# Kernel tuning notes

Hardware: AMD Instinct MI355X
Metric: run time of the kernel (lower is better)

## Reference

```python
import jax, jax.numpy as jnp
import numpy as np

B, S, D = 16, 512, 384
MAX_DUR = 16  # durations drawn from [0, 16)


def setup_inputs() -> dict:
    key = jax.random.key(0)
    k1, k2 = jax.random.split(key)
    hidden = jax.random.normal(k1, (B, S, D), dtype=jnp.float32)
    durations = jax.random.randint(k2, (B, S), 0, MAX_DUR, dtype=jnp.int32)
    return {"hidden": hidden, "durations": durations}


def reference(hidden, durations):
    # hidden: [B, S, D], durations: [B, S] int
    out_lengths = durations.sum(axis=1)              # [B]
    # NOTE: output length is data-dependent (matches torch eager semantics);
    # concretize it here. Under jit one would pass a static max_length instead.
    max_length = int(out_lengths.max())
    csum = jnp.cumsum(durations, axis=1)             # [B, S] inclusive cumsum
    pos = jnp.arange(max_length)                     # [L]
    # Output frame j of batch b copies token t where csum[b,t-1] <= j < csum[b,t]
    # (tokens with duration 0 are skipped automatically by side='right').
    idx = jax.vmap(lambda c: jnp.searchsorted(c, pos, side='right'))(csum)  # [B, L]
    idx = jnp.minimum(idx, hidden.shape[1] - 1)      # clamp padding region
    out = jnp.take_along_axis(hidden, idx[:, :, None], axis=1)  # [B, L, D]
    # zero out positions beyond each batch's expanded length (torch init zeros)
    valid = (pos[None, :] < out_lengths[:, None]).astype(hidden.dtype)  # [B, L]
    out = out * valid[:, :, None]
    return out, out_lengths
```

## Files before the change

### kernel.cpp

```cpp
#include <hip/hip_runtime.h>

#define NB 16
#define NS 512
#define ND 384
#define K4 (ND/4)
#define ROWS 16
#define NT 256

__global__ __launch_bounds__(NT) void length_regulator_fused(
    const float4* __restrict__ hidden4,
    const int*    __restrict__ dur,
    float4*       __restrict__ out4,
    float*        __restrict__ outLenF,
    int L)
{
    const int t = threadIdx.x;
    const int b = blockIdx.y;
    const int j0 = blockIdx.x * ROWS;

    __shared__ int wsum[NT / 64];
    __shared__ int rowTok[ROWS];

    if (t < ROWS) rowTok[t] = -1;

    int2 d2 = ((const int2*)(dur + b * NS))[t];
    int local = d2.x + d2.y;
    int lane = t & 63, wave = t >> 6;
    int x = local;
    #pragma unroll
    for (int off = 1; off < 64; off <<= 1) {
        int y = __shfl_up(x, off, 64);
        if (lane >= off) x += y;
    }
    if (lane == 63) wsum[wave] = x;
    __syncthreads();
    int wbase = 0, total = 0;
    #pragma unroll
    for (int w = 0; w < NT / 64; ++w) {
        int s = wsum[w];
        if (w < wave) wbase += s;
        total += s;
    }
    int excl = wbase + x - local;

    {
        int e0 = excl,        n0 = d2.x;
        int e1 = excl + d2.x, n1 = d2.y;
        int lo0 = max(e0, j0), hi0 = min(e0 + n0, j0 + ROWS);
        for (int j = lo0; j < hi0; ++j) rowTok[j - j0] = 2 * t;
        int lo1 = max(e1, j0), hi1 = min(e1 + n1, j0 + ROWS);
        for (int j = lo1; j < hi1; ++j) rowTok[j - j0] = 2 * t + 1;
    }
    __syncthreads();

    if (j0 == 0 && t == 0) outLenF[b] = (float)total;

    const size_t outBase = ((size_t)b * L + j0) * K4;
    const size_t hidBase = (size_t)b * NS * K4;
    #pragma unroll
    for (int i = t; i < ROWS * K4; i += NT) {
        int r = i / K4;
        int k = i - r * K4;
        if (j0 + r >= L) break;
        int g = rowTok[r];
        float4 v;
        if (g < 0) v = make_float4(0.f, 0.f, 0.f, 0.f);
        else       v = hidden4[hidBase + (size_t)g * K4 + k];
        out4[outBase + i] = v;
    }
}

extern "C" void kernel_launch(void* const* d_in, const int* in_sizes, int n_in,
                              void* d_out, int out_size, void* d_ws, size_t ws_size,
                              hipStream_t stream) {
    const float* hidden    = (const float*)d_in[0];
    const int*   durations = (const int*)d_in[1];
    float* out = (float*)d_out;

    int L = (out_size - NB) / (NB * ND);
    float* outLenF = out + (size_t)NB * L * ND;

    dim3 grid((L + ROWS - 1) / ROWS, NB);
    length_regulator_fused<<<grid, NT, 0, stream>>>(
        (const float4*)hidden, durations, (float4*)out, outLenF, L);
}
```

Measured before the change: 118.6 us.

## Split into map-building kernel plus gather kernel with nontemporal stores

Adds a one-block-per-batch kernel that computes the duration prefix sum once and writes a per-frame token index map into workspace. A second kernel then gathers rows by reading that map, covering 32 rows per block and using nontemporal stores for the output. This removes the redundant per-block prefix scan and its block barriers from the original fused kernel. In exchange it adds a second launch, a global round trip for the map, and a serialized map-writing phase in only 16 blocks. The old fused kernel is kept as a fallback when workspace is too small.

```diff
diff --git a/kernel.cpp b/kernel.cpp
--- a/kernel.cpp
+++ b/kernel.cpp
@@ -4,8 +4,91 @@
 #define NS 512
 #define ND 384
 #define K4 (ND/4)
-#define ROWS 16
 #define NT 256
+#define GROWS 32
+#define FROWS 16
+
+typedef float vf4 __attribute__((ext_vector_type(4)));
+
+__global__ __launch_bounds__(NT) void build_map(
+    const int* __restrict__ dur,
+    int*       __restrict__ rowMap,
+    float*     __restrict__ outLenF,
+    int L)
+{
+    const int t = threadIdx.x;
+    const int b = blockIdx.x;
+    __shared__ int wsum[NT / 64];
+
+    int2 d2 = ((const int2*)(dur + b * NS))[t];
+    int local = d2.x + d2.y;
+    int lane = t & 63, wave = t >> 6;
+    int x = local;
+    #pragma unroll
+    for (int off = 1; off < 64; off <<= 1) {
+        int y = __shfl_up(x, off, 64);
+        if (lane >= off) x += y;
+    }
+    if (lane == 63) wsum[wave] = x;
+    __syncthreads();
+    int wbase = 0, total = 0;
+    #pragma unroll
+    for (int w = 0; w < NT / 64; ++w) {
+        int s = wsum[w];
+        if (w < wave) wbase += s;
+        total += s;
+    }
+    int excl = wbase + x - local;
+
+    int* map = rowMap + (size_t)b * L;
+    int e0 = excl,        n0 = d2.x;
+    int e1 = excl + d2.x, n1 = d2.y;
+    for (int j = e0; j < e0 + n0; ++j) map[j] = 2 * t;
+    for (int j = e1; j < e1 + n1; ++j) map[j] = 2 * t + 1;
+    for (int j = total + t; j < L; j += NT) map[j] = -1;
+
+    if (t == 0) outLenF[b] = (float)total;
+}
+
+__global__ __launch_bounds__(NT) void gather_rows(
+    const vf4* __restrict__ hidden4,
+    const int* __restrict__ rowMap,
+    vf4*       __restrict__ out4,
+    int L)
+{
+    const int t  = threadIdx.x;
+    const int b  = blockIdx.y;
+    const int j0 = blockIdx.x * GROWS;
+    const int* __restrict__ map = rowMap + (size_t)b * L + j0;
+    const size_t outBase = ((size_t)b * L + j0) * K4;
+    const size_t hidBase = (size_t)b * NS * K4;
+
+    if (j0 + GROWS <= L) {
+        #pragma unroll
+        for (int i = 0; i < GROWS * K4 / NT; ++i) {
+            int idx = t + i * NT;
+            int r = idx / K4;
+            int k = idx - r * K4;
+            int g = map[r];
+            vf4 v = {0.f, 0.f, 0.f, 0.f};
+            if (g >= 0) v = hidden4[hidBase + (size_t)g * K4 + k];
+            __builtin_nontemporal_store(v, &out4[outBase + idx]);
+        }
+    } else {
+        const int rmax = L - j0;
+        #pragma unroll
+        for (int i = 0; i < GROWS * K4 / NT; ++i) {
+            int idx = t + i * NT;
+            int r = idx / K4;
+            int k = idx - r * K4;
+            if (r >= rmax) break;
+            int g = map[r];
+            vf4 v = {0.f, 0.f, 0.f, 0.f};
+            if (g >= 0) v = hidden4[hidBase + (size_t)g * K4 + k];
+            __builtin_nontemporal_store(v, &out4[outBase + idx]);
+        }
+    }
+}
 
 __global__ __launch_bounds__(NT) void length_regulator_fused(
     const float4* __restrict__ hidden4,
@@ -16,12 +99,12 @@
 {
     const int t = threadIdx.x;
     const int b = blockIdx.y;
-    const int j0 = blockIdx.x * ROWS;
+    const int j0 = blockIdx.x * FROWS;
 
     __shared__ int wsum[NT / 64];
-    __shared__ int rowTok[ROWS];
+    __shared__ int rowTok[FROWS];
 
-    if (t < ROWS) rowTok[t] = -1;
+    if (t < FROWS) rowTok[t] = -1;
 
     int2 d2 = ((const int2*)(dur + b * NS))[t];
     int local = d2.x + d2.y;
@@ -46,9 +129,9 @@
     {
         int e0 = excl,        n0 = d2.x;
         int e1 = excl + d2.x, n1 = d2.y;
-        int lo0 = max(e0, j0), hi0 = min(e0 + n0, j0 + ROWS);
+        int lo0 = max(e0, j0), hi0 = min(e0 + n0, j0 + FROWS);
         for (int j = lo0; j < hi0; ++j) rowTok[j - j0] = 2 * t;
-        int lo1 = max(e1, j0), hi1 = min(e1 + n1, j0 + ROWS);
+        int lo1 = max(e1, j0), hi1 = min(e1 + n1, j0 + FROWS);
         for (int j = lo1; j < hi1; ++j) rowTok[j - j0] = 2 * t + 1;
     }
     __syncthreads();
@@ -58,7 +141,7 @@
     const size_t outBase = ((size_t)b * L + j0) * K4;
     const size_t hidBase = (size_t)b * NS * K4;
     #pragma unroll
-    for (int i = t; i < ROWS * K4; i += NT) {
+    for (int i = t; i < FROWS * K4; i += NT) {
         int r = i / K4;
         int k = i - r * K4;
         if (j0 + r >= L) break;
@@ -80,7 +163,16 @@
     int L = (out_size - NB) / (NB * ND);
     float* outLenF = out + (size_t)NB * L * ND;
 
-    dim3 grid((L + ROWS - 1) / ROWS, NB);
-    length_regulator_fused<<<grid, NT, 0, stream>>>(
-        (const float4*)hidden, durations, (float4*)out, outLenF, L);
+    size_t mapBytes = (size_t)NB * L * sizeof(int);
+    if (ws_size >= mapBytes) {
+        int* rowMap = (int*)d_ws;
+        build_map<<<dim3(NB), NT, 0, stream>>>(durations, rowMap, outLenF, L);
+        dim3 grid((L + GROWS - 1) / GROWS, NB);
+        gather_rows<<<grid, NT, 0, stream>>>(
+            (const vf4*)hidden, rowMap, (vf4*)out, L);
+    } else {
+        dim3 grid((L + FROWS - 1) / FROWS, NB);
+        length_regulator_fused<<<grid, NT, 0, stream>>>(
+            (const float4*)hidden, durations, (float4*)out, outLenF, L);
+    }
 }
```

Result: slower. 128.5 us (+8.4%).
